# Optimization experiments

Measured on AMD Instinct MI355X. Metric: run time of the kernel, lower is better.

Reference implementation:

```python
import jax, jax.numpy as jnp
import numpy as np

N_NODES = 100000
N_EDGES = 1600000
IN_C = 128
HID = 128
LAT = 64
N_LAYERS = 3
N_GRAPHS = 1000


def setup_inputs() -> dict:
    key = jax.random.key(0)
    ks = jax.random.split(key, 16)
    x = jax.random.normal(ks[0], (N_NODES, IN_C), dtype=jnp.float32)
    edge_index = jax.random.randint(ks[1], (2, N_EDGES), 0, N_NODES, dtype=jnp.int64)
    batch = jnp.sort(jax.random.randint(ks[2], (N_NODES,), 0, N_GRAPHS, dtype=jnp.int64))
    s = 1.0 / np.sqrt(HID)
    # per-layer GIN MLP params (in_c == hidden for all layers since IN_C == HID)
    W1 = jax.random.normal(ks[3], (N_LAYERS, IN_C, HID), dtype=jnp.float32) * s
    b1 = jnp.zeros((N_LAYERS, HID), dtype=jnp.float32)
    W2 = jax.random.normal(ks[4], (N_LAYERS, HID, HID), dtype=jnp.float32) * s
    b2 = jnp.zeros((N_LAYERS, HID), dtype=jnp.float32)
    W_mu = jax.random.normal(ks[5], (HID, LAT), dtype=jnp.float32) * s
    b_mu = jnp.zeros((LAT,), dtype=jnp.float32)
    W_lv = jax.random.normal(ks[6], (HID, LAT), dtype=jnp.float32) * s
    b_lv = jnp.zeros((LAT,), dtype=jnp.float32)
    return {"x": x, "edge_index": edge_index, "batch": batch,
            "W1": W1, "b1": b1, "W2": W2, "b2": b2,
            "W_mu": W_mu, "b_mu": b_mu, "W_lv": W_lv, "b_lv": b_lv}


def reference(x, edge_index, batch, W1, b1, W2, b2, W_mu, b_mu, W_lv, b_lv):
    src, dst = edge_index[0], edge_index[1]
    h = x
    for i in range(N_LAYERS):
        # GINConv (eps=0): h' = MLP(h + sum_{j in N(i)} h_j); scatter-add over edges
        agg = h + jax.ops.segment_sum(h[src], dst, num_segments=N_NODES)
        h = jax.nn.relu(agg @ W1[i] + b1[i])
        h = jax.nn.relu(h @ W2[i] + b2[i])
        h = jax.nn.relu(h)  # extra ReLU in forward after conv (idempotent here)
    # global_add_pool: segment-sum nodes into graphs
    g = jax.ops.segment_sum(h, batch, num_segments=N_GRAPHS)  # [G, HID]
    mu = g @ W_mu + b_mu
    logvar = g @ W_lv + b_lv
    return (mu, logvar)
```

## Files before the change

kernel.cpp:

```cpp
#include <hip/hip_runtime.h>

#define N_NODES 100000
#define N_EDGES 1600000
#define HID 128
#define LAT 64
#define N_LAYERS 3
#define N_GRAPHS 1000
#define CAP 64
#define NBIN 391
#define MAXBIN 4608
#define ACHUNK 8192
#define ABLOCKS ((N_EDGES + ACHUNK - 1) / ACHUNK)
#define CVT_GRID 2048

typedef short bf16x8 __attribute__((ext_vector_type(8)));
typedef float f32x4 __attribute__((ext_vector_type(4)));

__device__ __forceinline__ float bf2f(unsigned short h) {
    union { unsigned int u; float f; } c;
    c.u = ((unsigned int)h) << 16;
    return c.f;
}
__device__ __forceinline__ unsigned short f2bf(float f) {
    union { float f; unsigned int u; } c;
    c.f = f;
    unsigned int u = c.u;
    return (unsigned short)((u + 0x7fffu + ((u >> 16) & 1u)) >> 16);
}
__device__ __forceinline__ unsigned int pack2(float a, float b) {
    return (unsigned int)f2bf(a) | ((unsigned int)f2bf(b) << 16);
}
__device__ __forceinline__ void addrow(float* acc, uint4 w) {
    acc[0] += bf2f((unsigned short)w.x); acc[1] += bf2f((unsigned short)(w.x >> 16));
    acc[2] += bf2f((unsigned short)w.y); acc[3] += bf2f((unsigned short)(w.y >> 16));
    acc[4] += bf2f((unsigned short)w.z); acc[5] += bf2f((unsigned short)(w.z >> 16));
    acc[6] += bf2f((unsigned short)w.w); acc[7] += bf2f((unsigned short)(w.w >> 16));
}

__global__ __launch_bounds__(256) void setup_kernel(const int* __restrict__ ei,
                                                    int* __restrict__ gcnt,
                                                    unsigned int* __restrict__ ebin,
                                                    const float* __restrict__ x,
                                                    unsigned short* __restrict__ xb,
                                                    const float* __restrict__ W1,
                                                    const float* __restrict__ W2,
                                                    unsigned short* __restrict__ Wt) {
    __shared__ unsigned int scount[NBIN];
    __shared__ unsigned int sfill[NBIN];
    int t = threadIdx.x;
    int blk = blockIdx.x;
    if (blk >= ABLOCKS) {
        int b2 = blk - ABLOCKS;
        if (b2 < 6) {
            const float* W = ((b2 & 1) ? W2 : W1) + (size_t)(b2 >> 1) * HID * HID;
            unsigned short* D = Wt + (size_t)b2 * HID * HID;
            for (int idx = t; idx < HID * HID; idx += 256) {
                int n = idx >> 7, k = idx & 127;
                D[n * HID + k] = f2bf(W[k * HID + n]);
            }
            return;
        }
        const int total = N_NODES * HID / 4;
        const int stride = CVT_GRID * 256;
        for (int i = (b2 - 6) * 256 + t; i < total; i += stride) {
            float4 v = ((const float4*)x)[i];
            ((uint2*)xb)[i] = make_uint2(pack2(v.x, v.y), pack2(v.z, v.w));
        }
        return;
    }
    int base = blk * ACHUNK;
    int n = N_EDGES - base;
    if (n > ACHUNK) n = ACHUNK;
    for (int i = t; i < NBIN; i += 256) scount[i] = 0u;
    __syncthreads();
    for (int i = t; i < n; i += 256) {
        int d = ei[N_EDGES + base + i];
        atomicAdd(&scount[d >> 8], 1u);
    }
    __syncthreads();
    for (int b = t; b < NBIN; b += 256) {
        unsigned int c = scount[b];
        sfill[b] = c ? (unsigned int)atomicAdd(&gcnt[b], (int)c) : 0u;
    }
    __syncthreads();
    for (int i = t; i < n; i += 256) {
        int s = ei[base + i];
        int d = ei[N_EDGES + base + i];
        int b = d >> 8;
        unsigned int pos = atomicAdd(&sfill[b], 1u);
        ebin[(size_t)b * MAXBIN + pos] = ((unsigned int)(d & 255) << 24) | (unsigned int)s;
    }
}

__global__ __launch_bounds__(256) void binB_kernel(const unsigned int* __restrict__ ebin,
                                                   const int* __restrict__ gcnt,
                                                   int* __restrict__ cnt,
                                                   int* __restrict__ csr) {
    __shared__ int lcsr[128][CAP];
    __shared__ int scnt[128];
    int blk = blockIdx.x;
    int b = blk >> 1;
    int half = blk & 1;
    int t = threadIdx.x;
    if (t < 128) scnt[t] = 0;
    __syncthreads();
    int c = gcnt[b];
    const unsigned int* src = ebin + (size_t)b * MAXBIN;
    for (int i = t; i < c; i += 256) {
        unsigned int e = src[i];
        int dl = (int)(e >> 24);
        if ((dl >> 7) == half) {
            int slot = atomicAdd(&scnt[dl & 127], 1);
            lcsr[dl & 127][slot] = (int)(e & 0xFFFFFFu);
        }
    }
    __syncthreads();
    int n0 = (b << 8) + (half << 7);
    if (t < 128 && n0 + t < N_NODES) cnt[n0 + t] = scnt[t];
    int nv = N_NODES - n0;
    if (nv > 128) nv = 128;
    if (nv < 0) nv = 0;
    int4* dst = (int4*)(csr + (size_t)n0 * CAP);
    const int4* ls = (const int4*)&lcsr[0][0];
    for (int i = t; i < nv * (CAP / 4); i += 256) dst[i] = ls[i];
}

__global__ __launch_bounds__(256) void gather_kernel(const unsigned short* __restrict__ h,
                                                     const int* __restrict__ cnt,
                                                     const int* __restrict__ csr,
                                                     unsigned short* __restrict__ agg) {
    int t = threadIdx.x;
    int node = blockIdx.x * 16 + (t >> 4);
    int q = t & 15;
    if (node >= N_NODES) return;
    const int* nl = csr + (size_t)node * CAP;
    int deg = cnt[node];
    float acc[8] = {0.f, 0.f, 0.f, 0.f, 0.f, 0.f, 0.f, 0.f};
    addrow(acc, *(const uint4*)(h + (size_t)node * HID + q * 8));
    int e = 0;
    for (; e + 8 <= deg; e += 8) {
        int s0 = nl[e], s1 = nl[e + 1], s2 = nl[e + 2], s3 = nl[e + 3];
        int s4 = nl[e + 4], s5 = nl[e + 5], s6 = nl[e + 6], s7 = nl[e + 7];
        uint4 w0 = *(const uint4*)(h + (size_t)s0 * HID + q * 8);
        uint4 w1 = *(const uint4*)(h + (size_t)s1 * HID + q * 8);
        uint4 w2 = *(const uint4*)(h + (size_t)s2 * HID + q * 8);
        uint4 w3 = *(const uint4*)(h + (size_t)s3 * HID + q * 8);
        uint4 w4 = *(const uint4*)(h + (size_t)s4 * HID + q * 8);
        uint4 w5 = *(const uint4*)(h + (size_t)s5 * HID + q * 8);
        uint4 w6 = *(const uint4*)(h + (size_t)s6 * HID + q * 8);
        uint4 w7 = *(const uint4*)(h + (size_t)s7 * HID + q * 8);
        addrow(acc, w0); addrow(acc, w1); addrow(acc, w2); addrow(acc, w3);
        addrow(acc, w4); addrow(acc, w5); addrow(acc, w6); addrow(acc, w7);
    }
    for (; e + 4 <= deg; e += 4) {
        int s0 = nl[e], s1 = nl[e + 1], s2 = nl[e + 2], s3 = nl[e + 3];
        uint4 w0 = *(const uint4*)(h + (size_t)s0 * HID + q * 8);
        uint4 w1 = *(const uint4*)(h + (size_t)s1 * HID + q * 8);
        uint4 w2 = *(const uint4*)(h + (size_t)s2 * HID + q * 8);
        uint4 w3 = *(const uint4*)(h + (size_t)s3 * HID + q * 8);
        addrow(acc, w0); addrow(acc, w1); addrow(acc, w2); addrow(acc, w3);
    }
    for (; e < deg; ++e) {
        addrow(acc, *(const uint4*)(h + (size_t)nl[e] * HID + q * 8));
    }
    uint4 o;
    o.x = pack2(acc[0], acc[1]);
    o.y = pack2(acc[2], acc[3]);
    o.z = pack2(acc[4], acc[5]);
    o.w = pack2(acc[6], acc[7]);
    *(uint4*)(agg + (size_t)node * HID + q * 8) = o;
}

__global__ __launch_bounds__(256) void mlp_kernel(const unsigned short* __restrict__ A,
                                                  const unsigned short* __restrict__ W1t,
                                                  const float* __restrict__ b1,
                                                  const unsigned short* __restrict__ W2t,
                                                  const float* __restrict__ b2,
                                                  unsigned short* __restrict__ out,
                                                  const int* __restrict__ batch,
                                                  float* __restrict__ gpool) {
    __shared__ unsigned short sA[64][136];
    __shared__ unsigned short sW[128][40];
    __shared__ float sb[128];
    __shared__ int sbatch[64];
    const int t = threadIdx.x;
    const int w = t >> 6;
    const int l = t & 63;
    const int lm = l & 15;
    const int quad = l >> 4;
    const int row0 = blockIdx.x * 64;

    for (int idx = t; idx < 1024; idx += 256) {
        int r = idx >> 4, c = idx & 15;
        int grow = row0 + r;
        uint4 v = make_uint4(0u, 0u, 0u, 0u);
        if (grow < N_NODES) v = *(const uint4*)(A + (size_t)grow * HID + c * 8);
        *(uint4*)&sA[r][c * 8] = v;
    }
    if (gpool && t < 64) {
        int n = row0 + t;
        sbatch[t] = (n < N_NODES) ? batch[n] : -1;
    }

    const unsigned short* Wt2[2] = {W1t, W2t};
    const float* bias[2] = {b1, b2};

    const int n_0 = t >> 2;
    const int n_1 = (t >> 2) + 64;
    const int kq = t & 3;
    uint4 rw0 = *(const uint4*)(W1t + (size_t)n_0 * HID + kq * 8);
    uint4 rw1 = *(const uint4*)(W1t + (size_t)n_1 * HID + kq * 8);

    for (int p = 0; p < 2; ++p) {
        if (t < 128) sb[t] = bias[p][t];
        f32x4 acc[8];
#pragma unroll
        for (int nt = 0; nt < 8; ++nt) acc[nt] = (f32x4){0.f, 0.f, 0.f, 0.f};

        for (int kc = 0; kc < 4; ++kc) {
            __syncthreads();
            *(uint4*)&sW[n_0][kq * 8] = rw0;
            *(uint4*)&sW[n_1][kq * 8] = rw1;
            __syncthreads();
            int s = (p << 2) + kc;
            if (s < 7) {
                int pn = (s + 1) >> 2, kn = (s + 1) & 3;
                const unsigned short* Wn = Wt2[pn];
                rw0 = *(const uint4*)(Wn + (size_t)n_0 * HID + kn * 32 + kq * 8);
                rw1 = *(const uint4*)(Wn + (size_t)n_1 * HID + kn * 32 + kq * 8);
            }
            bf16x8 a = *(const bf16x8*)&sA[w * 16 + lm][kc * 32 + quad * 8];
#pragma unroll
            for (int nt = 0; nt < 8; ++nt) {
                bf16x8 b = *(const bf16x8*)&sW[nt * 16 + lm][quad * 8];
                acc[nt] = __builtin_amdgcn_mfma_f32_16x16x32_bf16(a, b, acc[nt], 0, 0, 0);
            }
        }
        __syncthreads();
#pragma unroll
        for (int nt = 0; nt < 8; ++nt) {
            float bv = sb[nt * 16 + lm];
#pragma unroll
            for (int r = 0; r < 4; ++r) {
                int m = w * 16 + quad * 4 + r;
                float val = fmaxf(acc[nt][r] + bv, 0.f);
                sA[m][nt * 16 + lm] = f2bf(val);
            }
        }
        __syncthreads();
    }

    if (!gpool) {
        for (int idx = t; idx < 1024; idx += 256) {
            int r = idx >> 4, c = idx & 15;
            int grow = row0 + r;
            if (grow < N_NODES)
                *(uint4*)(out + (size_t)grow * HID + c * 8) = *(const uint4*)&sA[r][c * 8];
        }
    } else {
        int c = t & 127;
        int r0 = (t >> 7) * 32;
        float acc = 0.f;
        int cur = sbatch[r0];
        for (int r = r0; r < r0 + 32; ++r) {
            int b = sbatch[r];
            if (b < 0) break;
            if (b != cur) {
                atomicAdd(&gpool[(size_t)cur * HID + c], acc);
                acc = 0.f;
                cur = b;
            }
            acc += bf2f(sA[r][c]);
        }
        if (cur >= 0) atomicAdd(&gpool[(size_t)cur * HID + c], acc);
    }
}

__global__ __launch_bounds__(128) void head_kernel(const float* __restrict__ g,
                                                   const float* __restrict__ Wmu,
                                                   const float* __restrict__ bmu,
                                                   const float* __restrict__ Wlv,
                                                   const float* __restrict__ blv,
                                                   float* __restrict__ out) {
    __shared__ float sg[HID];
    int gi = blockIdx.x;
    sg[threadIdx.x] = g[(size_t)gi * HID + threadIdx.x];
    __syncthreads();
    int j = threadIdx.x & 63;
    bool is_lv = threadIdx.x >= 64;
    const float* W = is_lv ? Wlv : Wmu;
    float acc = is_lv ? blv[j] : bmu[j];
    for (int k = 0; k < HID; ++k) acc = fmaf(sg[k], W[k * LAT + j], acc);
    out[(is_lv ? (size_t)N_GRAPHS * LAT : 0) + (size_t)gi * LAT + j] = acc;
}

extern "C" void kernel_launch(void* const* d_in, const int* in_sizes, int n_in,
                              void* d_out, int out_size, void* d_ws, size_t ws_size,
                              hipStream_t stream) {
    const float* x     = (const float*)d_in[0];
    const int*   ei    = (const int*)d_in[1];
    const int*   batch = (const int*)d_in[2];
    const float* W1    = (const float*)d_in[3];
    const float* b1    = (const float*)d_in[4];
    const float* W2    = (const float*)d_in[5];
    const float* b2    = (const float*)d_in[6];
    const float* Wmu   = (const float*)d_in[7];
    const float* bmu   = (const float*)d_in[8];
    const float* Wlv   = (const float*)d_in[9];
    const float* blv   = (const float*)d_in[10];
    float* out = (float*)d_out;

    unsigned short* xb   = (unsigned short*)d_ws;
    unsigned short* agg  = xb + (size_t)N_NODES * HID;
    unsigned short* hbuf = agg + (size_t)N_NODES * HID;
    int* csr = (int*)(hbuf + (size_t)N_NODES * HID);
    unsigned int* ebin = (unsigned int*)(csr + (size_t)N_NODES * CAP);
    unsigned short* Wt = (unsigned short*)(ebin + (size_t)NBIN * MAXBIN);
    float* g  = (float*)(Wt + (size_t)6 * HID * HID);
    int* gcnt = (int*)(g + (size_t)N_GRAPHS * HID);
    int* cnt  = gcnt + NBIN + 1;

    hipMemsetAsync(g, 0, (size_t)N_GRAPHS * HID * sizeof(float) + (NBIN + 1) * sizeof(int),
                   stream);

    setup_kernel<<<ABLOCKS + 6 + CVT_GRID, 256, 0, stream>>>(ei, gcnt, ebin,
                                                             x, xb, W1, W2, Wt);
    binB_kernel<<<NBIN * 2, 256, 0, stream>>>(ebin, gcnt, cnt, csr);

    const unsigned short* hcur = xb;
    for (int i = 0; i < N_LAYERS; ++i) {
        bool last = (i == N_LAYERS - 1);
        gather_kernel<<<(N_NODES + 15) / 16, 256, 0, stream>>>(hcur, cnt, csr, agg);
        mlp_kernel<<<(N_NODES + 63) / 64, 256, 0, stream>>>(
            agg, Wt + (size_t)(2 * i) * HID * HID, b1 + (size_t)i * HID,
            Wt + (size_t)(2 * i + 1) * HID * HID, b2 + (size_t)i * HID, hbuf,
            batch, last ? g : nullptr);
        hcur = hbuf;
    }
    head_kernel<<<N_GRAPHS, 128, 0, stream>>>(g, Wmu, bmu, Wlv, blv, out);
}
```

Measured before the change: 408.9 us.

## Stage full W1 in shared memory and prefetch W2 into registers in MLP kernel

The fused two-layer MLP kernel now loads all of W1 into a larger shared tile up front, instead of streaming 32-wide k-chunks with two barriers per chunk. All of W2 is prefetched into registers while the first GEMM runs, then written to shared memory for the second GEMM. Biases are kept in registers. This cuts the barrier count and the per-chunk load/store stalls. In exchange, shared memory per block grows to about 52KB and register pressure rises, which may lower occupancy.

```diff
diff --git a/kernel.cpp b/kernel.cpp
--- a/kernel.cpp
+++ b/kernel.cpp
@@ -180,8 +180,7 @@
                                                   const int* __restrict__ batch,
                                                   float* __restrict__ gpool) {
     __shared__ unsigned short sA[64][136];
-    __shared__ unsigned short sW[128][40];
-    __shared__ float sb[128];
+    __shared__ unsigned short sW[128][136];
     __shared__ int sbatch[64];
     const int t = threadIdx.x;
     const int w = t >> 6;
@@ -197,58 +196,80 @@
         if (grow < N_NODES) v = *(const uint4*)(A + (size_t)grow * HID + c * 8);
         *(uint4*)&sA[r][c * 8] = v;
     }
+    for (int idx = t; idx < 2048; idx += 256) {
+        int r = idx >> 4, c = idx & 15;
+        *(uint4*)&sW[r][c * 8] = *(const uint4*)(W1t + (size_t)r * HID + c * 8);
+    }
     if (gpool && t < 64) {
         int n = row0 + t;
         sbatch[t] = (n < N_NODES) ? batch[n] : -1;
     }
-
-    const unsigned short* Wt2[2] = {W1t, W2t};
-    const float* bias[2] = {b1, b2};
-
-    const int n_0 = t >> 2;
-    const int n_1 = (t >> 2) + 64;
-    const int kq = t & 3;
-    uint4 rw0 = *(const uint4*)(W1t + (size_t)n_0 * HID + kq * 8);
-    uint4 rw1 = *(const uint4*)(W1t + (size_t)n_1 * HID + kq * 8);
-
-    for (int p = 0; p < 2; ++p) {
-        if (t < 128) sb[t] = bias[p][t];
-        f32x4 acc[8];
-#pragma unroll
-        for (int nt = 0; nt < 8; ++nt) acc[nt] = (f32x4){0.f, 0.f, 0.f, 0.f};
-
-        for (int kc = 0; kc < 4; ++kc) {
-            __syncthreads();
-            *(uint4*)&sW[n_0][kq * 8] = rw0;
-            *(uint4*)&sW[n_1][kq * 8] = rw1;
-            __syncthreads();
-            int s = (p << 2) + kc;
-            if (s < 7) {
-                int pn = (s + 1) >> 2, kn = (s + 1) & 3;
-                const unsigned short* Wn = Wt2[pn];
-                rw0 = *(const uint4*)(Wn + (size_t)n_0 * HID + kn * 32 + kq * 8);
-                rw1 = *(const uint4*)(Wn + (size_t)n_1 * HID + kn * 32 + kq * 8);
-            }
-            bf16x8 a = *(const bf16x8*)&sA[w * 16 + lm][kc * 32 + quad * 8];
-#pragma unroll
-            for (int nt = 0; nt < 8; ++nt) {
-                bf16x8 b = *(const bf16x8*)&sW[nt * 16 + lm][quad * 8];
-                acc[nt] = __builtin_amdgcn_mfma_f32_16x16x32_bf16(a, b, acc[nt], 0, 0, 0);
-            }
-        }
-        __syncthreads();
+    float bv1[8], bv2[8];
+#pragma unroll
+    for (int nt = 0; nt < 8; ++nt) {
+        bv1[nt] = b1[nt * 16 + lm];
+        bv2[nt] = b2[nt * 16 + lm];
+    }
+    __syncthreads();
+
+    uint4 rw[8];
+#pragma unroll
+    for (int i = 0; i < 8; ++i) {
+        int idx = t + i * 256;
+        int r = idx >> 4, c = idx & 15;
+        rw[i] = *(const uint4*)(W2t + (size_t)r * HID + c * 8);
+    }
+
+    f32x4 acc[8];
+#pragma unroll
+    for (int nt = 0; nt < 8; ++nt) acc[nt] = (f32x4){0.f, 0.f, 0.f, 0.f};
+#pragma unroll
+    for (int kc = 0; kc < 4; ++kc) {
+        bf16x8 a = *(const bf16x8*)&sA[w * 16 + lm][kc * 32 + quad * 8];
 #pragma unroll
         for (int nt = 0; nt < 8; ++nt) {
-            float bv = sb[nt * 16 + lm];
-#pragma unroll
-            for (int r = 0; r < 4; ++r) {
-                int m = w * 16 + quad * 4 + r;
-                float val = fmaxf(acc[nt][r] + bv, 0.f);
-                sA[m][nt * 16 + lm] = f2bf(val);
-            }
-        }
-        __syncthreads();
-    }
+            bf16x8 b = *(const bf16x8*)&sW[nt * 16 + lm][kc * 32 + quad * 8];
+            acc[nt] = __builtin_amdgcn_mfma_f32_16x16x32_bf16(a, b, acc[nt], 0, 0, 0);
+        }
+    }
+    __syncthreads();
+
+#pragma unroll
+    for (int nt = 0; nt < 8; ++nt) {
+#pragma unroll
+        for (int r = 0; r < 4; ++r) {
+            int m = w * 16 + quad * 4 + r;
+            sA[m][nt * 16 + lm] = f2bf(fmaxf(acc[nt][r] + bv1[nt], 0.f));
+        }
+    }
+#pragma unroll
+    for (int i = 0; i < 8; ++i) {
+        int idx = t + i * 256;
+        int r = idx >> 4, c = idx & 15;
+        *(uint4*)&sW[r][c * 8] = rw[i];
+    }
+    __syncthreads();
+
+#pragma unroll
+    for (int nt = 0; nt < 8; ++nt) acc[nt] = (f32x4){0.f, 0.f, 0.f, 0.f};
+#pragma unroll
+    for (int kc = 0; kc < 4; ++kc) {
+        bf16x8 a = *(const bf16x8*)&sA[w * 16 + lm][kc * 32 + quad * 8];
+#pragma unroll
+        for (int nt = 0; nt < 8; ++nt) {
+            bf16x8 b = *(const bf16x8*)&sW[nt * 16 + lm][kc * 32 + quad * 8];
+            acc[nt] = __builtin_amdgcn_mfma_f32_16x16x32_bf16(a, b, acc[nt], 0, 0, 0);
+        }
+    }
+#pragma unroll
+    for (int nt = 0; nt < 8; ++nt) {
+#pragma unroll
+        for (int r = 0; r < 4; ++r) {
+            int m = w * 16 + quad * 4 + r;
+            sA[m][nt * 16 + lm] = f2bf(fmaxf(acc[nt][r] + bv2[nt], 0.f));
+        }
+    }
+    __syncthreads();
 
     if (!gpool) {
         for (int idx = t; idx < 1024; idx += 256) {
@@ -260,19 +281,19 @@
     } else {
         int c = t & 127;
         int r0 = (t >> 7) * 32;
-        float acc = 0.f;
+        float acc3 = 0.f;
         int cur = sbatch[r0];
         for (int r = r0; r < r0 + 32; ++r) {
             int b = sbatch[r];
             if (b < 0) break;
             if (b != cur) {
-                atomicAdd(&gpool[(size_t)cur * HID + c], acc);
-                acc = 0.f;
+                atomicAdd(&gpool[(size_t)cur * HID + c], acc3);
+                acc3 = 0.f;
                 cur = b;
             }
-            acc += bf2f(sA[r][c]);
-        }
-        if (cur >= 0) atomicAdd(&gpool[(size_t)cur * HID + c], acc);
+            acc3 += bf2f(sA[r][c]);
+        }
+        if (cur >= 0) atomicAdd(&gpool[(size_t)cur * HID + c], acc3);
     }
 }
 
```

Result: slower. 445.5 us (+9.0%).
